# Kernel tuning notes

Measured on AMD Instinct MI355X. Metric: run time of the kernel, lower is better.

## Reference

```python
import jax, jax.numpy as jnp
import numpy as np

DIM = 128
WS = 7          # window size
NH = 4          # num heads
N = WS * WS     # tokens per window = 49
GRID = 56       # 224/4 token grid -> 8x8 = 64 windows per image
NUM_WIN = (GRID // WS) ** 2  # 64
IMG_B = 64
SCALE = (DIM // NH) ** -0.5


def _relative_position_index():
    coords = np.stack(np.meshgrid(np.arange(WS), np.arange(WS), indexing='ij'))  # (2,WS,WS)
    flat = coords.reshape(2, -1)                         # (2, N)
    rel = flat[:, :, None] - flat[:, None, :]            # (2, N, N)
    rel = rel.transpose(1, 2, 0).astype(np.int32)        # (N, N, 2)
    rel[:, :, 0] += WS - 1
    rel[:, :, 1] += WS - 1
    rel[:, :, 0] *= 2 * WS - 1
    return jnp.asarray(rel.sum(-1))                      # (N, N) int32


def _shift_mask():
    # Swin shifted-window attention mask: shift = WS // 2, off-group pairs get -100.
    shift = WS // 2
    img = np.zeros((GRID, GRID), dtype=np.int32)
    cnt = 0
    segs = (slice(0, -WS), slice(-WS, -shift), slice(-shift, None))
    for hs in segs:
        for ws_ in segs:
            img[hs, ws_] = cnt
            cnt += 1
    # window partition -> (NUM_WIN, N)
    w = img.reshape(GRID // WS, WS, GRID // WS, WS).transpose(0, 2, 1, 3).reshape(NUM_WIN, N)
    diff = w[:, :, None] - w[:, None, :]
    return jnp.asarray(np.where(diff != 0, -100.0, 0.0).astype(np.float32))  # (NUM_WIN, N, N)


def setup_inputs() -> dict:
    key = jax.random.key(0)
    ks = jax.random.split(key, 6)
    B = IMG_B * NUM_WIN  # 4096
    x = jax.random.normal(ks[0], (B, N, DIM), dtype=jnp.float32)
    qkv_w = jax.random.normal(ks[1], (3 * DIM, DIM), dtype=jnp.float32) * (DIM ** -0.5)
    qkv_b = jnp.zeros((3 * DIM,), dtype=jnp.float32)
    proj_w = jax.random.normal(ks[2], (DIM, DIM), dtype=jnp.float32) * (DIM ** -0.5)
    proj_b = jnp.zeros((DIM,), dtype=jnp.float32)
    rel_bias_table = jax.random.normal(ks[3], ((2 * WS - 1) ** 2, NH), dtype=jnp.float32) * 0.02
    return {
        'x': x,
        'mask': _shift_mask(),
        'qkv_w': qkv_w,
        'qkv_b': qkv_b,
        'proj_w': proj_w,
        'proj_b': proj_b,
        'rel_bias_table': rel_bias_table,
        'rel_index': _relative_position_index(),
    }


def reference(x, mask, qkv_w, qkv_b, proj_w, proj_b, rel_bias_table, rel_index):
    B, n, C = x.shape
    hd = C // NH
    qkv = (x @ qkv_w.T + qkv_b).reshape(B, n, 3, NH, hd)
    q = qkv[:, :, 0].transpose(0, 2, 1, 3) * SCALE   # (B, H, N, hd)
    k = qkv[:, :, 1].transpose(0, 2, 1, 3)
    v = qkv[:, :, 2].transpose(0, 2, 1, 3)
    attn = jnp.einsum('bhnd,bhmd->bhnm', q, k)       # (B, H, N, N)
    bias = rel_bias_table[rel_index.reshape(-1)].reshape(n, n, NH).transpose(2, 0, 1)
    attn = attn + bias[None]
    nW = mask.shape[0]
    attn = attn.reshape(B // nW, nW, NH, n, n) + mask[None, :, None]
    attn = jax.nn.softmax(attn.reshape(B, NH, n, n), axis=-1)
    out = jnp.einsum('bhnm,bhmd->bhnd', attn, v).transpose(0, 2, 1, 3).reshape(B, n, C)
    return out @ proj_w.T + proj_b
```

## Files before the change

### kernel.cpp

```cpp
#include <hip/hip_runtime.h>


#define NTOK  49
#define DIMC  128
#define NBLK  4096
#define SCALE 0.17677669529663687f
#define LOG2E 1.4426950408889634f
#define NMASK -144.26950408889634f

typedef __attribute__((ext_vector_type(8))) short bf16x8;
typedef __attribute__((ext_vector_type(4))) float f32x4;

#define WS_QKVW 0
#define WS_PROJW 49152
#define WS_BIAS  65536

#define XP_OFF 0
#define Q_OFF  6272
#define K_OFF  12544
#define VB_OFF 18816
#define SMEM_TOT 27008

#define SWZ(r, c) ((r) * 128 + ((c) ^ (((r) & 7) << 3)))

__device__ __forceinline__ unsigned int pkbf2(float f0, float f1) {
    union { float f; unsigned int i; } a, b; a.f = f0; b.f = f1;
    return __builtin_amdgcn_perm(b.i + 0x8000u, a.i + 0x8000u, 0x07060302u);
}
__device__ __forceinline__ unsigned short f2b_r(float f) {
    union { float f; unsigned int i; } v; v.f = f;
    return (unsigned short)((v.i + 0x8000u) >> 16);
}
__device__ __forceinline__ float b2f_lo(unsigned int u) {
    union { unsigned int i; float f; } v; v.i = u << 16; return v.f;
}
__device__ __forceinline__ float b2f_hi(unsigned int u) {
    union { unsigned int i; float f; } v; v.i = u & 0xFFFF0000u; return v.f;
}
__device__ __forceinline__ float exp2_hw(float x) {
    float r; asm("v_exp_f32 %0, %1" : "=v"(r) : "v"(x)); return r;
}

__device__ __forceinline__ int seg3(int c) { return (c < 49) ? 0 : ((c < 53) ? 1 : 2); }

__global__ __launch_bounds__(256)
void prep(const float* __restrict__ qkv_w, const float* __restrict__ proj_w,
          const float* __restrict__ bias_t, const int* __restrict__ rel_idx,
          unsigned short* __restrict__ ws)
{
    int idx = blockIdx.x * 256 + threadIdx.x;
    if (idx < 8192) {
        int base = idx * 8;
        const float* sp = (base < 49152) ? (qkv_w + base) : (proj_w + (base - 49152));
        float sc = (base < 16384) ? (SCALE * LOG2E) : 1.0f;
        float4 a = *(const float4*)sp;
        float4 b = *(const float4*)(sp + 4);
        uint4 u;
        u.x = pkbf2(a.x * sc, a.y * sc);
        u.y = pkbf2(a.z * sc, a.w * sc);
        u.z = pkbf2(b.x * sc, b.y * sc);
        u.w = pkbf2(b.z * sc, b.w * sc);
        *(uint4*)(ws + base) = u;
    } else {
        int i = idx - 8192;
        int reg = i & 3, lane = (i >> 2) & 63, nt = (i >> 8) & 3,
            mt = (i >> 10) & 3, h = (i >> 12) & 3;
        int row = mt * 16 + (lane >> 4) * 4 + reg;
        int col = nt * 16 + (lane & 15);
        float v = 0.f;
        if (row < NTOK && col < NTOK)
            v = bias_t[rel_idx[row * NTOK + col] * 4 + h] * LOG2E;
        ws[WS_BIAS + i] = f2b_r(v);
    }
}

__global__ __launch_bounds__(512, 4)
void win_attn(const float* __restrict__ x,
              const float* __restrict__ qkv_b,
              const float* __restrict__ proj_b,
              const unsigned short* __restrict__ ws,
              float* __restrict__ out)
{
    __shared__ unsigned short smem[SMEM_TOT];
    const int b    = blockIdx.x;
    const int w    = b & 63;
    const int tid  = threadIdx.x;
    const int wv   = tid >> 6;
    const int lane = tid & 63;
    const int qg   = lane >> 4;
    const int l15  = lane & 15;

    {
        const float4* xg = (const float4*)(x + (size_t)b * (NTOK * DIMC));
        #pragma unroll
        for (int it = 0; it < 4; it++) {
            int i = tid + it * 512;
            if (i < NTOK * DIMC / 4) {
                float4 v = xg[i];
                int row = i >> 5, col = (i & 31) * 4;
                uint2 u; u.x = pkbf2(v.x, v.y); u.y = pkbf2(v.z, v.w);
                *(uint2*)(smem + XP_OFF + SWZ(row, col)) = u;
            }
        }
    }
    __syncthreads();

    {
        const unsigned short* qw = ws + WS_QKVW;
        const int h2 = wv >> 1;
        const int dhalf = wv & 1;
        const int dh = dhalf * 16 + l15;
        #pragma unroll
        for (int pp = 0; pp < 3; pp++) {
            const int j = (pp * 8 + wv) * 16 + l15;
            bf16x8 bfr[4];
            #pragma unroll
            for (int ks_ = 0; ks_ < 4; ks_++)
                bfr[ks_] = *(const bf16x8*)(qw + j * DIMC + ks_ * 32 + qg * 8);
            const float bias = (pp == 0) ? qkv_b[j] * (SCALE * LOG2E) : qkv_b[j];
            #pragma unroll
            for (int mt = 0; mt < 4; mt++) {
                int ar = mt * 16 + l15; if (ar > 48) ar = 48;
                f32x4 acc = { bias, bias, bias, bias };
                #pragma unroll
                for (int ks_ = 0; ks_ < 4; ks_++) {
                    bf16x8 afm = *(const bf16x8*)(smem + XP_OFF + SWZ(ar, ks_ * 32 + qg * 8));
                    acc = __builtin_amdgcn_mfma_f32_16x16x32_bf16(afm, bfr[ks_], acc, 0, 0, 0);
                }
                if (pp == 0) {
                    #pragma unroll
                    for (int r = 0; r < 4; r++) {
                        int row = mt * 16 + qg * 4 + r;
                        if (row < NTOK)
                            smem[Q_OFF + SWZ(row, h2 * 32 + dh)] = f2b_r(acc[r]);
                    }
                } else if (pp == 1) {
                    #pragma unroll
                    for (int r = 0; r < 4; r++) {
                        int row = mt * 16 + qg * 4 + r;
                        if (row < NTOK)
                            smem[K_OFF + SWZ(row, h2 * 32 + dh)] = f2b_r(acc[r]);
                    }
                } else {
                    int ks2 = mt >> 1;
                    int qgp = (mt & 1) * 2 + (qg >> 1);
                    int j0  = (qg & 1) * 4;
                    uint2 u; u.x = pkbf2(acc[0], acc[1]); u.y = pkbf2(acc[2], acc[3]);
                    *(uint2*)(smem + VB_OFF + h2 * 2048 + ks2 * 1024 + dhalf * 512
                              + qgp * 128 + l15 * 8 + j0) = u;
                }
            }
        }
    }
    __syncthreads();

    const int g  = wv >> 2;
    const int st = wv & 3;
    const int r0 = st * 16;
    const int wy = w >> 3, wx = w & 7;
    int grow[4];
    #pragma unroll
    for (int r = 0; r < 4; r++) {
        int t = r0 + qg * 4 + r;
        int ty = (t * 9363) >> 16, tx = t - ty * 7;
        grow[r] = seg3(wy * 7 + ty) * 3 + seg3(wx * 7 + tx);
    }
    int arq = r0 + l15; if (arq > 48) arq = 48;

    #pragma unroll
    for (int hh = 0; hh < 2; hh++) {
        const int h = 2 * g + hh;
        const bf16x8 aq = *(const bf16x8*)(smem + Q_OFF + SWZ(arq, h * 32 + qg * 8));
        float sv[4][4];
        #pragma unroll
        for (int nt = 0; nt < 4; nt++) {
            int krow = nt * 16 + l15; if (krow > 48) krow = 48;
            bf16x8 bk = *(const bf16x8*)(smem + K_OFF + SWZ(krow, h * 32 + qg * 8));
            f32x4 z = { 0.f, 0.f, 0.f, 0.f };
            f32x4 c = __builtin_amdgcn_mfma_f32_16x16x32_bf16(aq, bk, z, 0, 0, 0);
            uint2 bb = *(const uint2*)(ws + WS_BIAS + (((h * 4 + st) * 4 + nt) * 64 + lane) * 4);
            int t = nt * 16 + l15;
            int ty = (t * 9363) >> 16, tx = t - ty * 7;
            int gcol = seg3(wy * 7 + ty) * 3 + seg3(wx * 7 + tx);
            bool vc = t < NTOK;
            float bv[4] = { b2f_lo(bb.x), b2f_hi(bb.x), b2f_lo(bb.y), b2f_hi(bb.y) };
            #pragma unroll
            for (int r = 0; r < 4; r++) {
                float v = c[r] + bv[r] + ((grow[r] == gcol) ? 0.f : NMASK);
                sv[nt][r] = vc ? v : -1e30f;
            }
        }
        float inv[4];
        #pragma unroll
        for (int r = 0; r < 4; r++) {
            float mx = fmaxf(fmaxf(sv[0][r], sv[1][r]), fmaxf(sv[2][r], sv[3][r]));
            mx = fmaxf(mx, __shfl_xor(mx, 1));
            mx = fmaxf(mx, __shfl_xor(mx, 2));
            mx = fmaxf(mx, __shfl_xor(mx, 4));
            mx = fmaxf(mx, __shfl_xor(mx, 8));
            float sum = 0.f;
            #pragma unroll
            for (int nt = 0; nt < 4; nt++) {
                float e = exp2_hw(sv[nt][r] - mx);
                sv[nt][r] = e; sum += e;
            }
            sum += __shfl_xor(sum, 1);
            sum += __shfl_xor(sum, 2);
            sum += __shfl_xor(sum, 4);
            sum += __shfl_xor(sum, 8);
            inv[r] = __builtin_amdgcn_rcpf(sum);
        }
        #pragma unroll
        for (int nt = 0; nt < 4; nt++)
            #pragma unroll
            for (int r = 0; r < 4; r++) {
                int row = r0 + qg * 4 + r;
                if (row < NTOK)
                    smem[XP_OFF + SWZ(row, g * 64 + nt * 16 + l15)] = f2b_r(sv[nt][r]);
            }
        f32x4 accO[2] = { { 0.f, 0.f, 0.f, 0.f }, { 0.f, 0.f, 0.f, 0.f } };
        #pragma unroll
        for (int ks2 = 0; ks2 < 2; ks2++) {
            bf16x8 ap = *(const bf16x8*)(smem + XP_OFF + SWZ(arq, g * 64 + ks2 * 32 + qg * 8));
            #pragma unroll
            for (int nt2 = 0; nt2 < 2; nt2++) {
                bf16x8 bvv = *(const bf16x8*)(smem + VB_OFF + h * 2048 + ks2 * 1024 + nt2 * 512 + lane * 8);
                accO[nt2] = __builtin_amdgcn_mfma_f32_16x16x32_bf16(ap, bvv, accO[nt2], 0, 0, 0);
            }
        }
        #pragma unroll
        for (int nt2 = 0; nt2 < 2; nt2++)
            #pragma unroll
            for (int r = 0; r < 4; r++) {
                int row = r0 + qg * 4 + r;
                if (row < NTOK)
                    smem[Q_OFF + SWZ(row, h * 32 + nt2 * 16 + l15)] =
                        f2b_r(accO[nt2][r] * inv[r]);
            }
    }
    __syncthreads();

    {
        const int mt = wv & 3, jh = wv >> 2;
        int ar = mt * 16 + l15; if (ar > 48) ar = 48;
        bf16x8 ad[4];
        #pragma unroll
        for (int ks_ = 0; ks_ < 4; ks_++)
            ad[ks_] = *(const bf16x8*)(smem + Q_OFF + SWZ(ar, ks_ * 32 + qg * 8));
        const unsigned short* pw = ws + WS_PROJW;
        float* ob = out + (size_t)b * (NTOK * DIMC);
        #pragma unroll
        for (int jt2 = 0; jt2 < 4; jt2++) {
            const int j = jh * 64 + jt2 * 16 + l15;
            bf16x8 bfr[4];
            #pragma unroll
            for (int ks_ = 0; ks_ < 4; ks_++)
                bfr[ks_] = *(const bf16x8*)(pw + j * DIMC + ks_ * 32 + qg * 8);
            const float pb = proj_b[j];
            f32x4 acc = { pb, pb, pb, pb };
            #pragma unroll
            for (int ks_ = 0; ks_ < 4; ks_++)
                acc = __builtin_amdgcn_mfma_f32_16x16x32_bf16(ad[ks_], bfr[ks_], acc, 0, 0, 0);
            #pragma unroll
            for (int r = 0; r < 4; r++) {
                int row = mt * 16 + qg * 4 + r;
                if (row < NTOK) ob[row * DIMC + j] = acc[r];
            }
        }
    }
}

extern "C" void kernel_launch(void* const* d_in, const int* in_sizes, int n_in,
                              void* d_out, int out_size, void* d_ws, size_t ws_size,
                              hipStream_t stream) {
    const float* x      = (const float*)d_in[0];
    const float* qkv_w  = (const float*)d_in[2];
    const float* qkv_b  = (const float*)d_in[3];
    const float* proj_w = (const float*)d_in[4];
    const float* proj_b = (const float*)d_in[5];
    const float* bias_t = (const float*)d_in[6];
    const int*   relidx = (const int*)d_in[7];
    float*       outp   = (float*)d_out;
    unsigned short* ws  = (unsigned short*)d_ws;

    prep<<<96, 256, 0, stream>>>(qkv_w, proj_w, bias_t, relidx, ws);
    win_attn<<<NBLK, 512, 0, stream>>>(x, qkv_b, proj_b, ws, outp);
}
```

Measured before the change: 298.2 us.

## Load x directly into MFMA registers and store V transposed with padded stride

Drops the LDS staging of the input tile and its barrier. Each wave now reads its x rows from global memory, converts them to bf16 in registers, and reuses them across the Q, K and V projections. QKV weight fragments are re-read inside the row-tile loop. V is stored as a transposed, 56-stride layout with a zeroed tail, and the P@V B-operand loads are adapted to it. This trades the LDS round-trip and one sync for redundant global and L2 reads of x (every wave reads the full tile) and more weight loads. It also relies on padded or neighbouring V entries being multiplied by zero probabilities.

```diff
diff --git a/kernel.cpp b/kernel.cpp
--- a/kernel.cpp
+++ b/kernel.cpp
@@ -15,11 +15,12 @@
 #define WS_PROJW 49152
 #define WS_BIAS  65536
 
-#define XP_OFF 0
+#define P_OFF  0
 #define Q_OFF  6272
 #define K_OFF  12544
 #define VB_OFF 18816
-#define SMEM_TOT 27008
+#define VB_STRIDE 56
+#define SMEM_TOT 25992
 
 #define SWZ(r, c) ((r) * 128 + ((c) ^ (((r) & 7) << 3)))
 
@@ -90,42 +91,45 @@
     const int qg   = lane >> 4;
     const int l15  = lane & 15;
 
-    {
-        const float4* xg = (const float4*)(x + (size_t)b * (NTOK * DIMC));
-        #pragma unroll
-        for (int it = 0; it < 4; it++) {
-            int i = tid + it * 512;
-            if (i < NTOK * DIMC / 4) {
-                float4 v = xg[i];
-                int row = i >> 5, col = (i & 31) * 4;
-                uint2 u; u.x = pkbf2(v.x, v.y); u.y = pkbf2(v.z, v.w);
-                *(uint2*)(smem + XP_OFF + SWZ(row, col)) = u;
-            }
-        }
-    }
-    __syncthreads();
+    if (tid == 0) {
+        uint4 z = { 0u, 0u, 0u, 0u };
+        *(uint4*)(smem + VB_OFF + 127 * VB_STRIDE + VB_STRIDE) = z;
+    }
 
     {
         const unsigned short* qw = ws + WS_QKVW;
         const int h2 = wv >> 1;
         const int dhalf = wv & 1;
         const int dh = dhalf * 16 + l15;
+        const float* xb = x + (size_t)b * (NTOK * DIMC);
+        float bias_pp[3];
         #pragma unroll
         for (int pp = 0; pp < 3; pp++) {
-            const int j = (pp * 8 + wv) * 16 + l15;
-            bf16x8 bfr[4];
-            #pragma unroll
-            for (int ks_ = 0; ks_ < 4; ks_++)
-                bfr[ks_] = *(const bf16x8*)(qw + j * DIMC + ks_ * 32 + qg * 8);
-            const float bias = (pp == 0) ? qkv_b[j] * (SCALE * LOG2E) : qkv_b[j];
-            #pragma unroll
-            for (int mt = 0; mt < 4; mt++) {
-                int ar = mt * 16 + l15; if (ar > 48) ar = 48;
-                f32x4 acc = { bias, bias, bias, bias };
+            int j = (pp * 8 + wv) * 16 + l15;
+            bias_pp[pp] = (pp == 0) ? qkv_b[j] * (SCALE * LOG2E) : qkv_b[j];
+        }
+        #pragma unroll
+        for (int mt = 0; mt < 4; mt++) {
+            int ar = mt * 16 + l15; if (ar > 48) ar = 48;
+            const float* xr = xb + ar * DIMC;
+            bf16x8 af[4];
+            #pragma unroll
+            for (int ks_ = 0; ks_ < 4; ks_++) {
+                float4 lo = *(const float4*)(xr + ks_ * 32 + qg * 8);
+                float4 hi = *(const float4*)(xr + ks_ * 32 + qg * 8 + 4);
+                union { uint4 u; bf16x8 v; } cv;
+                cv.u.x = pkbf2(lo.x, lo.y); cv.u.y = pkbf2(lo.z, lo.w);
+                cv.u.z = pkbf2(hi.x, hi.y); cv.u.w = pkbf2(hi.z, hi.w);
+                af[ks_] = cv.v;
+            }
+            #pragma unroll
+            for (int pp = 0; pp < 3; pp++) {
+                const int j = (pp * 8 + wv) * 16 + l15;
+                f32x4 acc = { bias_pp[pp], bias_pp[pp], bias_pp[pp], bias_pp[pp] };
                 #pragma unroll
                 for (int ks_ = 0; ks_ < 4; ks_++) {
-                    bf16x8 afm = *(const bf16x8*)(smem + XP_OFF + SWZ(ar, ks_ * 32 + qg * 8));
-                    acc = __builtin_amdgcn_mfma_f32_16x16x32_bf16(afm, bfr[ks_], acc, 0, 0, 0);
+                    bf16x8 bfr = *(const bf16x8*)(qw + j * DIMC + ks_ * 32 + qg * 8);
+                    acc = __builtin_amdgcn_mfma_f32_16x16x32_bf16(af[ks_], bfr, acc, 0, 0, 0);
                 }
                 if (pp == 0) {
                     #pragma unroll
@@ -142,12 +146,11 @@
                             smem[K_OFF + SWZ(row, h2 * 32 + dh)] = f2b_r(acc[r]);
                     }
                 } else {
-                    int ks2 = mt >> 1;
-                    int qgp = (mt & 1) * 2 + (qg >> 1);
-                    int j0  = (qg & 1) * 4;
-                    uint2 u; u.x = pkbf2(acc[0], acc[1]); u.y = pkbf2(acc[2], acc[3]);
-                    *(uint2*)(smem + VB_OFF + h2 * 2048 + ks2 * 1024 + dhalf * 512
-                              + qgp * 128 + l15 * 8 + j0) = u;
+                    int tokbase = mt * 16 + qg * 4;
+                    if (tokbase <= 52) {
+                        uint2 u; u.x = pkbf2(acc[0], acc[1]); u.y = pkbf2(acc[2], acc[3]);
+                        *(uint2*)(smem + VB_OFF + (h2 * 32 + dh) * VB_STRIDE + tokbase) = u;
+                    }
                 }
             }
         }
@@ -216,15 +219,16 @@
             for (int r = 0; r < 4; r++) {
                 int row = r0 + qg * 4 + r;
                 if (row < NTOK)
-                    smem[XP_OFF + SWZ(row, g * 64 + nt * 16 + l15)] = f2b_r(sv[nt][r]);
+                    smem[P_OFF + SWZ(row, g * 64 + nt * 16 + l15)] = f2b_r(sv[nt][r]);
             }
         f32x4 accO[2] = { { 0.f, 0.f, 0.f, 0.f }, { 0.f, 0.f, 0.f, 0.f } };
         #pragma unroll
         for (int ks2 = 0; ks2 < 2; ks2++) {
-            bf16x8 ap = *(const bf16x8*)(smem + XP_OFF + SWZ(arq, g * 64 + ks2 * 32 + qg * 8));
+            bf16x8 ap = *(const bf16x8*)(smem + P_OFF + SWZ(arq, g * 64 + ks2 * 32 + qg * 8));
             #pragma unroll
             for (int nt2 = 0; nt2 < 2; nt2++) {
-                bf16x8 bvv = *(const bf16x8*)(smem + VB_OFF + h * 2048 + ks2 * 1024 + nt2 * 512 + lane * 8);
+                bf16x8 bvv = *(const bf16x8*)(smem + VB_OFF
+                              + (h * 32 + nt2 * 16 + l15) * VB_STRIDE + ks2 * 32 + qg * 8);
                 accO[nt2] = __builtin_amdgcn_mfma_f32_16x16x32_bf16(ap, bvv, accO[nt2], 0, 0, 0);
             }
         }
```

New measurement: 486.1 us. 63.0% more time.
